# Optimization experiments

Hardware: AMD Instinct MI355X
Metric: run time of the kernel (lower is better)

The kernel has to match this reference:

```python
import jax, jax.numpy as jnp
import numpy as np

K = 5
BN_EPS = 1e-5


def _knn(xyz1, xyz2, embedding_lens):
    # squared pairwise distances [B, N, S]
    d2 = (jnp.sum(xyz1 ** 2, -1)[:, :, None]
          + jnp.sum(xyz2 ** 2, -1)[:, None, :]
          - 2.0 * jnp.einsum('bnc,bsc->bns', xyz1, xyz2))
    S = xyz2.shape[1]
    valid2 = jnp.arange(S)[None, :] < embedding_lens[:, None]  # [B, S]
    d2 = jnp.where(valid2[:, None, :], d2, jnp.float32(1e10))
    neg, idx = jax.lax.top_k(-d2, K)  # K smallest distances
    return -neg, idx  # squared dists [B,N,K], indices [B,N,K]


def _masked_bn(x, mask_f, gamma, beta):
    # x: [B, N, C]; mask_f: [B, N, 1] float; stats over valid positions only
    cnt = jnp.sum(mask_f)
    mean = jnp.sum(x * mask_f, axis=(0, 1)) / cnt
    var = jnp.sum(((x - mean) ** 2) * mask_f, axis=(0, 1)) / cnt
    return (x - mean) * jax.lax.rsqrt(var + BN_EPS) * gamma + beta


def setup_inputs() -> dict:
    key = jax.random.key(0)
    ks = jax.random.split(key, 8)
    B, N, S, D1, D2 = 16, 2048, 512, 384, 384
    xyz1 = jax.random.normal(ks[0], (B, N, 3), jnp.float32)
    xyz2 = jax.random.normal(ks[1], (B, S, 3), jnp.float32)
    points1 = jax.random.normal(ks[2], (B, N, D1), jnp.float32)
    points2 = jax.random.normal(ks[3], (B, S, D2), jnp.float32)
    point_lens = jax.random.randint(ks[4], (B,), N // 2, N + 1).astype(jnp.int32)
    embedding_lens = jax.random.randint(ks[5], (B,), S // 2, S + 1).astype(jnp.int32)
    point_mask = jnp.arange(N)[None, :] < point_lens[:, None]  # [B, N] bool
    Cin = D1 + D2
    W0 = jax.random.normal(ks[6], (768, Cin), jnp.float32) * (1.0 / np.sqrt(Cin))
    W1 = jax.random.normal(ks[7], (384, 768), jnp.float32) * (1.0 / np.sqrt(768))
    return dict(xyz1=xyz1, xyz2=xyz2, points1=points1, points2=points2,
                point_lens=point_lens, embedding_lens=embedding_lens,
                point_mask=point_mask,
                W0=W0, g0=jnp.ones((768,), jnp.float32), b0=jnp.zeros((768,), jnp.float32),
                W1=W1, g1=jnp.ones((384,), jnp.float32), b1=jnp.zeros((384,), jnp.float32))


def reference(xyz1, xyz2, points1, points2, point_lens, embedding_lens,
              point_mask, W0, g0, b0, W1, g1, b1):
    B, N, _ = xyz1.shape
    D2 = points2.shape[-1]
    dists, idx = _knn(xyz1[..., :3], xyz2, embedding_lens)
    eps = jnp.finfo(dists.dtype).eps
    dist_recip = 1.0 / (dists + eps)                    # [B, N, K]
    weight = dist_recip / jnp.sum(dist_recip, axis=2, keepdims=True)
    # masked gather: points2[b, idx[b,n,k], :] -> [B, N, K, D2]
    gathered = jnp.take_along_axis(points2, idx.reshape(B, N * K)[..., None],
                                   axis=1).reshape(B, N, K, D2)
    interp = jnp.sum(gathered * weight[..., None], axis=2)  # [B, N, D2]
    x = jnp.concatenate([points1, interp], axis=-1)          # [B, N, D1+D2]
    mask_f = point_mask.astype(x.dtype)[..., None]           # [B, N, 1]
    for W, g, b in ((W0, g0, b0), (W1, g1, b1)):
        x = jnp.einsum('bnc,dc->bnd', x, W)  # 1x1 conv, no bias
        x = jax.nn.relu(_masked_bn(x, mask_f, g, b))
    return x
```

## Files before the change

### kernel.cpp

```cpp
#include <hip/hip_runtime.h>
#include <cstdint>
#include <cstddef>

typedef unsigned short u16;
typedef __bf16 bf16x8 __attribute__((ext_vector_type(8)));
typedef float    f32x4 __attribute__((ext_vector_type(4)));
typedef unsigned int u32x4 __attribute__((ext_vector_type(4)));

constexpr int BB   = 16;
constexpr int NN   = 2048;
constexpr int SS   = 512;
constexpr int DD   = 384;
constexpr int CIN  = 768;
constexpr int HID  = 768;
constexpr int OUTC = 384;
constexpr int MROWS = BB * NN;
constexpr float KNN_EPS = 1.1920929e-07f;
constexpr float BN_EPS  = 1e-5f;

constexpr size_t OFF_W0B  = 0;
constexpr size_t OFF_W1B  = OFF_W0B  + (size_t)HID*CIN*2;
constexpr size_t OFF_IDX  = OFF_W1B  + (size_t)OUTC*HID*2;
constexpr size_t OFF_WGT  = OFF_IDX  + (size_t)MROWS*5*4;
constexpr size_t OFF_SUM1 = OFF_WGT  + (size_t)MROWS*5*4;
constexpr size_t OFF_SUM2 = OFF_SUM1 + (size_t)HID*2*4;
constexpr size_t OFF_COEF1= OFF_SUM2 + (size_t)OUTC*2*4;
constexpr size_t OFF_COEF2= OFF_COEF1+ (size_t)HID*2*4;
constexpr size_t OFF_XCAT = OFF_COEF2+ (size_t)OUTC*2*4;
constexpr size_t OFF_H1   = OFF_XCAT + (size_t)MROWS*CIN*2;

__device__ inline float bf2f(u16 u){ unsigned int i = ((unsigned int)u)<<16; float f; __builtin_memcpy(&f,&i,4); return f; }
__device__ inline u16 f2bf(float f){ unsigned int x; __builtin_memcpy(&x,&f,4);
  unsigned int r = (x + 0x7fffu + ((x>>16)&1u)) >> 16; return (u16)r; }

__device__ inline void async16(const void* g, void* l){
  __builtin_amdgcn_global_load_lds((const __attribute__((address_space(1))) void*)g,
                                   (__attribute__((address_space(3))) void*)l, 16, 0, 0);
}

__global__ void cvtw_kernel(const float* __restrict__ W0, const float* __restrict__ W1,
                            u16* __restrict__ W0b, u16* __restrict__ W1b){
  int t = blockIdx.x*256 + threadIdx.x;
  if (t < HID*CIN)  W0b[t] = f2bf(W0[t]);
  if (t < OUTC*HID) W1b[t] = f2bf(W1[t]);
}

__global__ __launch_bounds__(256) void knn_kernel(const float* __restrict__ xyz1,
                                                  const float* __restrict__ xyz2,
                                                  const int* __restrict__ elens,
                                                  int* __restrict__ idxO, float* __restrict__ wO){
  __shared__ f32x4 sp[SS];
  const int tid = threadIdx.x;
  const int wv = tid >> 6, lane = tid & 63;
  const int wg = blockIdx.x*4 + wv;
  const int b = wg >> 11;
  const int n = wg & (NN-1);
  for (int s = tid; s < SS; s += 256){
    float x = xyz2[((size_t)b*SS + s)*3 + 0];
    float y = xyz2[((size_t)b*SS + s)*3 + 1];
    float z = xyz2[((size_t)b*SS + s)*3 + 2];
    f32x4 v; v[0]=x; v[1]=y; v[2]=z; v[3]=x*x+y*y+z*z;
    sp[s]=v;
  }
  __syncthreads();
  const size_t qoff = ((size_t)b*NN + n)*3;
  const float qx = xyz1[qoff+0], qy = xyz1[qoff+1], qz = xyz1[qoff+2];
  const float qq = qx*qx + qy*qy + qz*qz;
  const int Sl = elens[b];

  float d0=1e30f,d1=1e30f,d2v=1e30f,d3=1e30f,d4=1e30f;
  int   i0=0,i1=0,i2=0,i3=0,i4=0;
  #pragma unroll
  for (int j=0;j<8;j++){
    const int s = lane + j*64;
    f32x4 v = sp[s];
    float d = (s < Sl) ? (qq + v[3] - 2.f*(qx*v[0] + qy*v[1] + qz*v[2])) : 1e30f;
    bool lt4=d<d4, lt3=d<d3, lt2=d<d2v, lt1=d<d1, lt0=d<d0;
    float nd4 = lt3 ? d3 : (lt4 ? d : d4); int ni4 = lt3 ? i3 : (lt4 ? s : i4);
    float nd3 = lt2 ? d2v: (lt3 ? d : d3); int ni3 = lt2 ? i2 : (lt3 ? s : i3);
    float nd2 = lt1 ? d1 : (lt2 ? d : d2v);int ni2 = lt1 ? i1 : (lt2 ? s : i2);
    float nd1 = lt0 ? d0 : (lt1 ? d : d1); int ni1 = lt0 ? i0 : (lt1 ? s : i1);
    float nd0 = lt0 ? d  : d0;             int ni0 = lt0 ? s  : i0;
    d4=nd4;i4=ni4; d3=nd3;i3=ni3; d2v=nd2;i2=ni2; d1=nd1;i1=ni1; d0=nd0;i0=ni0;
  }
  float outd[5]; int outi[5];
  #pragma unroll
  for (int r=0;r<5;r++){
    float bd = d0; int bs = i0;
    #pragma unroll
    for (int m=1;m<64;m<<=1){
      float od = __shfl_xor(bd, m, 64);
      int   os = __shfl_xor(bs, m, 64);
      if (od < bd || (od == bd && os < bs)){ bd = od; bs = os; }
    }
    outd[r]=bd; outi[r]=bs;
    if (d0 == bd && i0 == bs){ d0=d1;i0=i1; d1=d2v;i1=i2; d2v=d3;i2=i3; d3=d4;i3=i4; d4=1e30f;i4=0; }
  }
  if (lane == 0){
    float r0=1.f/(outd[0]+KNN_EPS), r1=1.f/(outd[1]+KNN_EPS), r2=1.f/(outd[2]+KNN_EPS),
          r3=1.f/(outd[3]+KNN_EPS), r4=1.f/(outd[4]+KNN_EPS);
    float inv = 1.f/(r0+r1+r2+r3+r4);
    size_t base = (size_t)wg*5;
    idxO[base+0]=outi[0]; idxO[base+1]=outi[1]; idxO[base+2]=outi[2]; idxO[base+3]=outi[3]; idxO[base+4]=outi[4];
    wO[base+0]=r0*inv; wO[base+1]=r1*inv; wO[base+2]=r2*inv; wO[base+3]=r3*inv; wO[base+4]=r4*inv;
  }
}

__global__ __launch_bounds__(384) void xcat_kernel(const float* __restrict__ p1,
                                                   const float* __restrict__ p2,
                                                   const int* __restrict__ idx,
                                                   const float* __restrict__ wgt,
                                                   u16* __restrict__ xcat){
  const int c = threadIdx.x;
  const int rowbase = blockIdx.x*8;
  for (int i=0;i<8;i++){
    const int row = rowbase + i;
    const int b = row >> 11;
    float v1 = p1[(size_t)row*DD + c];
    xcat[(size_t)row*CIN + c] = f2bf(v1);
    float acc = 0.f;
    size_t ib = (size_t)row*5;
    #pragma unroll
    for (int k=0;k<5;k++){
      int id = idx[ib+k]; float w = wgt[ib+k];
      acc += w * p2[((size_t)b*SS + id)*DD + c];
    }
    xcat[(size_t)row*CIN + DD + c] = f2bf(acc);
  }
}

template<bool OUT_BF16, int GX>
__global__ __launch_bounds__(256, 4) void gemm8p_kernel(const u16* __restrict__ A,
                                                        const u16* __restrict__ Bw,
                                                        void* __restrict__ Cout,
                                                        const int* __restrict__ plen,
                                                        float* __restrict__ sums){
  constexpr int K   = 768;
  constexpr int NC  = GX*128;
  constexpr int NT  = K/32;
  constexpr int NWG = GX*256;
  constexpr int CPX = NWG/8;
  __shared__ u16 Ash[2][128*32];
  __shared__ u16 Bsh[2][128*32];
  const int tid  = threadIdx.x;
  const int lane = tid & 63, wv = tid >> 6;
  const int wr = wv >> 1, wc = wv & 1;
  const int l15 = lane & 15, l16 = lane >> 4;
  const int swz = (l15 >> 1) & 3;

  const int logical = (blockIdx.x & 7)*CPX + (blockIdx.x >> 3);
  const int bn = logical % GX, bm = logical / GX;

  const int srow = tid >> 2;
  const int sk4  = (tid & 3) ^ ((tid >> 3) & 3);
  const u16* gA = A  + (size_t)(bm*128 + srow)*K + sk4*8;
  const u16* gB = Bw + (size_t)(bn*128 + srow)*K + sk4*8;
  const int dst0 = (wv*64)*16;
  const int dst1 = (256 + wv*64)*16;

  auto stageA = [&](int tt, int bi){
    async16(gA + tt*32,        (char*)&Ash[bi][0] + dst0);
    async16(gA + tt*32 + 64*K, (char*)&Ash[bi][0] + dst1);
  };
  auto stageB = [&](int tt, int bi){
    async16(gB + tt*32,        (char*)&Bsh[bi][0] + dst0);
    async16(gB + tt*32 + 64*K, (char*)&Bsh[bi][0] + dst1);
  };

  int aoff[4], boff[4];
  #pragma unroll
  for (int m=0;m<4;m++) aoff[m] = (wr*64 + m*16 + l15)*32 + ((l16 ^ swz) << 3);
  #pragma unroll
  for (int n=0;n<4;n++) boff[n] = (wc*64 + n*16 + l15)*32 + ((l16 ^ swz) << 3);

  f32x4 acc[4][4] = {};

  stageA(0,0); stageB(0,0); stageA(1,1); stageB(1,1);
  asm volatile("s_waitcnt vmcnt(4)" ::: "memory");
  __builtin_amdgcn_s_barrier();
  __builtin_amdgcn_sched_barrier(0);

  for (int t=0; t<NT; ++t){
    const int cur = t & 1;
    const int tt = (t+2 < NT) ? (t+2) : (NT-1);
    bf16x8 af0 = *reinterpret_cast<const bf16x8*>(&Ash[cur][aoff[0]]);
    bf16x8 af1 = *reinterpret_cast<const bf16x8*>(&Ash[cur][aoff[1]]);
    bf16x8 af2 = *reinterpret_cast<const bf16x8*>(&Ash[cur][aoff[2]]);
    bf16x8 af3 = *reinterpret_cast<const bf16x8*>(&Ash[cur][aoff[3]]);
    bf16x8 bv0 = *reinterpret_cast<const bf16x8*>(&Bsh[cur][boff[0]]);
    bf16x8 bv1 = *reinterpret_cast<const bf16x8*>(&Bsh[cur][boff[1]]);
    asm volatile("s_waitcnt lgkmcnt(0)" ::: "memory");
    __builtin_amdgcn_s_barrier();
    __builtin_amdgcn_sched_barrier(0);
    stageA(tt, cur);
    __builtin_amdgcn_s_setprio(1);
    acc[0][0] = __builtin_amdgcn_mfma_f32_16x16x32_bf16(af0, bv0, acc[0][0], 0,0,0);
    acc[1][0] = __builtin_amdgcn_mfma_f32_16x16x32_bf16(af1, bv0, acc[1][0], 0,0,0);
    acc[2][0] = __builtin_amdgcn_mfma_f32_16x16x32_bf16(af2, bv0, acc[2][0], 0,0,0);
    acc[3][0] = __builtin_amdgcn_mfma_f32_16x16x32_bf16(af3, bv0, acc[3][0], 0,0,0);
    acc[0][1] = __builtin_amdgcn_mfma_f32_16x16x32_bf16(af0, bv1, acc[0][1], 0,0,0);
    acc[1][1] = __builtin_amdgcn_mfma_f32_16x16x32_bf16(af1, bv1, acc[1][1], 0,0,0);
    acc[2][1] = __builtin_amdgcn_mfma_f32_16x16x32_bf16(af2, bv1, acc[2][1], 0,0,0);
    acc[3][1] = __builtin_amdgcn_mfma_f32_16x16x32_bf16(af3, bv1, acc[3][1], 0,0,0);
    __builtin_amdgcn_s_setprio(0);
    bf16x8 bv2 = *reinterpret_cast<const bf16x8*>(&Bsh[cur][boff[2]]);
    bf16x8 bv3 = *reinterpret_cast<const bf16x8*>(&Bsh[cur][boff[3]]);
    asm volatile("s_waitcnt lgkmcnt(0)" ::: "memory");
    __builtin_amdgcn_s_barrier();
    __builtin_amdgcn_sched_barrier(0);
    stageB(tt, cur);
    __builtin_amdgcn_s_setprio(1);
    acc[0][2] = __builtin_amdgcn_mfma_f32_16x16x32_bf16(af0, bv2, acc[0][2], 0,0,0);
    acc[1][2] = __builtin_amdgcn_mfma_f32_16x16x32_bf16(af1, bv2, acc[1][2], 0,0,0);
    acc[2][2] = __builtin_amdgcn_mfma_f32_16x16x32_bf16(af2, bv2, acc[2][2], 0,0,0);
    acc[3][2] = __builtin_amdgcn_mfma_f32_16x16x32_bf16(af3, bv2, acc[3][2], 0,0,0);
    acc[0][3] = __builtin_amdgcn_mfma_f32_16x16x32_bf16(af0, bv3, acc[0][3], 0,0,0);
    acc[1][3] = __builtin_amdgcn_mfma_f32_16x16x32_bf16(af1, bv3, acc[1][3], 0,0,0);
    acc[2][3] = __builtin_amdgcn_mfma_f32_16x16x32_bf16(af2, bv3, acc[2][3], 0,0,0);
    acc[3][3] = __builtin_amdgcn_mfma_f32_16x16x32_bf16(af3, bv3, acc[3][3], 0,0,0);
    __builtin_amdgcn_s_setprio(0);
    asm volatile("s_waitcnt vmcnt(4)" ::: "memory");
    __builtin_amdgcn_s_barrier();
    __builtin_amdgcn_sched_barrier(0);
  }
  asm volatile("s_waitcnt vmcnt(0)" ::: "memory");
  __syncthreads();

  #pragma unroll
  for (int m=0;m<4;m++){
    int r0 = bm*128 + wr*64 + m*16 + l16*4;
    #pragma unroll
    for (int n=0;n<4;n++){
      int c = bn*128 + wc*64 + n*16 + l15;
      #pragma unroll
      for (int r=0;r<4;r++){
        size_t off = (size_t)(r0+r)*NC + c;
        if (OUT_BF16) ((u16*)Cout)[off] = f2bf(acc[m][n][r]);
        else          ((float*)Cout)[off] = acc[m][n][r];
      }
    }
  }

  const int pl = plen[bm >> 4];
  const int rbase = (bm & 15)*128 + wr*64 + l16*4;
  float cs[4] = {0.f,0.f,0.f,0.f}, cs2[4] = {0.f,0.f,0.f,0.f};
  #pragma unroll
  for (int m=0;m<4;m++){
    #pragma unroll
    for (int r=0;r<4;r++){
      if (rbase + m*16 + r < pl){
        #pragma unroll
        for (int n=0;n<4;n++){
          float v = acc[m][n][r];
          cs[n] += v; cs2[n] += v*v;
        }
      }
    }
  }
  #pragma unroll
  for (int n=0;n<4;n++){
    cs[n]  += __shfl_xor(cs[n], 16, 64);  cs[n]  += __shfl_xor(cs[n], 32, 64);
    cs2[n] += __shfl_xor(cs2[n], 16, 64); cs2[n] += __shfl_xor(cs2[n], 32, 64);
  }
  float* lsum = (float*)&Ash[0][0];
  lsum[tid] = 0.f;
  __syncthreads();
  if (l16 == 0){
    #pragma unroll
    for (int n=0;n<4;n++){
      int col = wc*64 + n*16 + l15;
      atomicAdd(&lsum[col], cs[n]);
      atomicAdd(&lsum[128 + col], cs2[n]);
    }
  }
  __syncthreads();
  if (tid < 128)       atomicAdd(&sums[bn*128 + tid], lsum[tid]);
  else                 atomicAdd(&sums[NC + bn*128 + (tid-128)], lsum[tid]);
}

__global__ void coef_kernel(const float* __restrict__ sums, const int* __restrict__ plen,
                            const float* __restrict__ g, const float* __restrict__ bta,
                            float* __restrict__ coef, int C){
  int c = threadIdx.x;
  if (c >= C) return;
  float cnt = 0.f;
  for (int b=0;b<BB;b++) cnt += (float)plen[b];
  float mean = sums[c] / cnt;
  float var  = sums[C + c] / cnt - mean*mean;
  var = fmaxf(var, 0.f);
  float a = g[c] * rsqrtf(var + BN_EPS);
  coef[c] = a;
  coef[C + c] = bta[c] - mean*a;
}

__global__ __launch_bounds__(256) void bnrelu_kernel(const u16* __restrict__ H,
                                                     const float* __restrict__ coef,
                                                     u16* __restrict__ Z){
  size_t t = (size_t)blockIdx.x*256 + threadIdx.x;
  size_t f = t*8;
  int c = (int)(f % (size_t)HID);
  u32x4 v = *reinterpret_cast<const u32x4*>(H + f);
  u32x4 o;
  #pragma unroll
  for (int j=0;j<4;j++){
    float lo = bf2f((u16)(v[j] & 0xffffu));
    float hi = bf2f((u16)(v[j] >> 16));
    lo = fmaxf(lo*coef[c+2*j]   + coef[HID+c+2*j],   0.f);
    hi = fmaxf(hi*coef[c+2*j+1] + coef[HID+c+2*j+1], 0.f);
    o[j] = (unsigned int)f2bf(lo) | ((unsigned int)f2bf(hi) << 16);
  }
  *reinterpret_cast<u32x4*>(Z + f) = o;
}

__global__ __launch_bounds__(256) void final_kernel(float* __restrict__ Y,
                                                    const float* __restrict__ coef){
  size_t t = (size_t)blockIdx.x*256 + threadIdx.x;
  size_t f = t*4;
  int c = (int)(f % (size_t)OUTC);
  f32x4 v = *reinterpret_cast<const f32x4*>(Y + f);
  #pragma unroll
  for (int j=0;j<4;j++)
    v[j] = fmaxf(v[j]*coef[c+j] + coef[OUTC+c+j], 0.f);
  *reinterpret_cast<f32x4*>(Y + f) = v;
}

extern "C" void kernel_launch(void* const* d_in, const int* in_sizes, int n_in,
                              void* d_out, int out_size, void* d_ws, size_t ws_size,
                              hipStream_t stream){
  (void)in_sizes; (void)n_in; (void)out_size; (void)ws_size;
  const float* xyz1 = (const float*)d_in[0];
  const float* xyz2 = (const float*)d_in[1];
  const float* p1   = (const float*)d_in[2];
  const float* p2   = (const float*)d_in[3];
  const int*   plen = (const int*)d_in[4];
  const int*   elen = (const int*)d_in[5];
  const float* W0   = (const float*)d_in[7];
  const float* g0   = (const float*)d_in[8];
  const float* b0   = (const float*)d_in[9];
  const float* W1   = (const float*)d_in[10];
  const float* g1   = (const float*)d_in[11];
  const float* b1   = (const float*)d_in[12];
  float* out = (float*)d_out;
  char*  ws  = (char*)d_ws;

  u16*   W0b  = (u16*)  (ws + OFF_W0B);
  u16*   W1b  = (u16*)  (ws + OFF_W1B);
  int*   idxb = (int*)  (ws + OFF_IDX);
  float* wgtb = (float*)(ws + OFF_WGT);
  float* sum1 = (float*)(ws + OFF_SUM1);
  float* sum2 = (float*)(ws + OFF_SUM2);
  float* coef1= (float*)(ws + OFF_COEF1);
  float* coef2= (float*)(ws + OFF_COEF2);
  u16*   xcat = (u16*)  (ws + OFF_XCAT);
  u16*   h1   = (u16*)  (ws + OFF_H1);

  hipMemsetAsync(ws + OFF_SUM1, 0, (size_t)(HID*2 + OUTC*2)*4, stream);

  cvtw_kernel<<<(HID*CIN + 255)/256, 256, 0, stream>>>(W0, W1, W0b, W1b);
  knn_kernel<<<MROWS/4, 256, 0, stream>>>(xyz1, xyz2, elen, idxb, wgtb);
  xcat_kernel<<<MROWS/8, 384, 0, stream>>>(p1, p2, idxb, wgtb, xcat);

  gemm8p_kernel<true, 6><<<6*256, 256, 0, stream>>>(xcat, W0b, h1, plen, sum1);
  coef_kernel<<<1, HID, 0, stream>>>(sum1, plen, g0, b0, coef1, HID);

  bnrelu_kernel<<<(size_t)MROWS*HID/8/256, 256, 0, stream>>>(h1, coef1, xcat);

  gemm8p_kernel<false, 3><<<3*256, 256, 0, stream>>>(xcat, W1b, out, plen, sum2);
  coef_kernel<<<1, OUTC, 0, stream>>>(sum2, plen, g1, b1, coef2, OUTC);
  final_kernel<<<(size_t)MROWS*OUTC/4/256, 256, 0, stream>>>(out, coef2);
}
```

Before: 196.9 us.

## Fuse BN+ReLU of first layer into second GEMM's A-tile loading

Removes the standalone bnrelu pass over the 32768x768 hidden tensor. The second GEMM now loads A through registers, applies the per-channel scale/shift and ReLU, and writes the result to shared memory, while B is still staged asynchronously. This saves a full read and write of the bf16 hidden activations. In exchange the A path becomes a register round-trip with extra VALU work inside the pipelined loop. The first GEMM also gets its own specialization with launch bounds raised to 5 waves.

Result: slower. 231.2 us (+17.4%).

```diff
diff --git a/kernel.cpp b/kernel.cpp
--- a/kernel.cpp
+++ b/kernel.cpp
@@ -129,14 +129,14 @@
   }
 }
 
-template<bool OUT_BF16, int GX>
-__global__ __launch_bounds__(256, 4) void gemm8p_kernel(const u16* __restrict__ A,
-                                                        const u16* __restrict__ Bw,
-                                                        void* __restrict__ Cout,
-                                                        const int* __restrict__ plen,
-                                                        float* __restrict__ sums){
-  constexpr int K   = 768;
-  constexpr int NC  = GX*128;
+__global__ __launch_bounds__(256, 5) void gemm1_kernel(const u16* __restrict__ A,
+                                                       const u16* __restrict__ Bw,
+                                                       u16* __restrict__ Cout,
+                                                       const int* __restrict__ plen,
+                                                       float* __restrict__ sums){
+  constexpr int K   = CIN;
+  constexpr int NC  = HID;
+  constexpr int GX  = NC/128;
   constexpr int NT  = K/32;
   constexpr int NWG = GX*256;
   constexpr int CPX = NWG/8;
@@ -233,11 +233,8 @@
     for (int n=0;n<4;n++){
       int c = bn*128 + wc*64 + n*16 + l15;
       #pragma unroll
-      for (int r=0;r<4;r++){
-        size_t off = (size_t)(r0+r)*NC + c;
-        if (OUT_BF16) ((u16*)Cout)[off] = f2bf(acc[m][n][r]);
-        else          ((float*)Cout)[off] = acc[m][n][r];
-      }
+      for (int r=0;r<4;r++)
+        Cout[(size_t)(r0+r)*NC + c] = f2bf(acc[m][n][r]);
     }
   }
 
@@ -293,23 +290,189 @@
   coef[C + c] = bta[c] - mean*a;
 }
 
-__global__ __launch_bounds__(256) void bnrelu_kernel(const u16* __restrict__ H,
-                                                     const float* __restrict__ coef,
-                                                     u16* __restrict__ Z){
-  size_t t = (size_t)blockIdx.x*256 + threadIdx.x;
-  size_t f = t*8;
-  int c = (int)(f % (size_t)HID);
-  u32x4 v = *reinterpret_cast<const u32x4*>(H + f);
-  u32x4 o;
-  #pragma unroll
-  for (int j=0;j<4;j++){
-    float lo = bf2f((u16)(v[j] & 0xffffu));
-    float hi = bf2f((u16)(v[j] >> 16));
-    lo = fmaxf(lo*coef[c+2*j]   + coef[HID+c+2*j],   0.f);
-    hi = fmaxf(hi*coef[c+2*j+1] + coef[HID+c+2*j+1], 0.f);
-    o[j] = (unsigned int)f2bf(lo) | ((unsigned int)f2bf(hi) << 16);
-  }
-  *reinterpret_cast<u32x4*>(Z + f) = o;
+__global__ __launch_bounds__(256, 4) void gemm2f_kernel(const u16* __restrict__ A,
+                                                        const u16* __restrict__ Bw,
+                                                        float* __restrict__ Cout,
+                                                        const int* __restrict__ plen,
+                                                        float* __restrict__ sums,
+                                                        const float* __restrict__ cf){
+  constexpr int K   = HID;
+  constexpr int NC  = OUTC;
+  constexpr int GX  = NC/128;
+  constexpr int NT  = K/32;
+  constexpr int NWG = (MROWS/128)*GX;
+  constexpr int CPX = NWG/8;
+  __shared__ u16 Ash[2][4096];
+  __shared__ u16 Bsh[2][4096];
+  const int tid  = threadIdx.x;
+  const int lane = tid & 63, wv = tid >> 6;
+  const int wr = wv >> 1, wc = wv & 1;
+  const int l15 = lane & 15, l16 = lane >> 4;
+  const int swz = (l15 >> 1) & 3;
+
+  const int logical = (blockIdx.x & 7)*CPX + (blockIdx.x >> 3);
+  const int bn = logical % GX, bm = logical / GX;
+
+  const int srow = tid >> 2;
+  const int sk4  = (tid & 3) ^ ((tid >> 3) & 3);
+  const u16* gB  = Bw + (size_t)(bn*128 + srow)*K + sk4*8;
+  const u16* gA0 = A  + (size_t)(bm*128 + srow)*K + sk4*8;
+  const u16* gA1 = gA0 + (size_t)64*K;
+
+  const int dst0 = (wv*64)*16;
+  const int dst1 = (256 + wv*64)*16;
+  auto stageB = [&](int tt, int bi){
+    async16(gB + tt*32,        (char*)&Bsh[bi][0] + dst0);
+    async16(gB + tt*32 + 64*K, (char*)&Bsh[bi][0] + dst1);
+  };
+
+  u32x4 ha0, ha1, hb0, hb1;
+  auto loadA = [&](int tt, u32x4& r0, u32x4& r1){
+    r0 = *reinterpret_cast<const u32x4*>(gA0 + tt*32);
+    r1 = *reinterpret_cast<const u32x4*>(gA1 + tt*32);
+  };
+  auto bnw1 = [&](int nb, int tt, const u32x4& v, int uoff){
+    const int k0 = tt*32 + sk4*8;
+    float av[8], bv[8];
+    *reinterpret_cast<f32x4*>(av)   = *reinterpret_cast<const f32x4*>(cf + k0);
+    *reinterpret_cast<f32x4*>(av+4) = *reinterpret_cast<const f32x4*>(cf + k0 + 4);
+    *reinterpret_cast<f32x4*>(bv)   = *reinterpret_cast<const f32x4*>(cf + K + k0);
+    *reinterpret_cast<f32x4*>(bv+4) = *reinterpret_cast<const f32x4*>(cf + K + k0 + 4);
+    u32x4 o;
+    #pragma unroll
+    for (int q=0;q<4;q++){
+      float lo = bf2f((u16)(v[q] & 0xffffu));
+      float hi = bf2f((u16)(v[q] >> 16));
+      lo = fmaxf(lo*av[2*q]   + bv[2*q],   0.f);
+      hi = fmaxf(hi*av[2*q+1] + bv[2*q+1], 0.f);
+      o[q] = (unsigned int)f2bf(lo) | ((unsigned int)f2bf(hi) << 16);
+    }
+    *reinterpret_cast<u32x4*>(&Ash[nb][uoff]) = o;
+  };
+  auto bnwrite = [&](int nb, int tt, const u32x4& v0, const u32x4& v1){
+    bnw1(nb, tt, v0, tid*8);
+    bnw1(nb, tt, v1, 2048 + tid*8);
+  };
+
+  int aoff[4], boff[4];
+  #pragma unroll
+  for (int m=0;m<4;m++) aoff[m] = (wr*64 + m*16 + l15)*32 + ((l16 ^ swz) << 3);
+  #pragma unroll
+  for (int n=0;n<4;n++) boff[n] = (wc*64 + n*16 + l15)*32 + ((l16 ^ swz) << 3);
+
+  f32x4 acc[4][4] = {};
+
+  loadA(0, ha0, ha1);
+  stageB(0, 0);
+  __builtin_amdgcn_sched_barrier(0);
+  bnwrite(0, 0, ha0, ha1);
+  __builtin_amdgcn_sched_barrier(0);
+  loadA(1, hb0, hb1);
+  __builtin_amdgcn_sched_barrier(0);
+  asm volatile("s_waitcnt vmcnt(2)" ::: "memory");
+  asm volatile("s_waitcnt lgkmcnt(0)" ::: "memory");
+  __builtin_amdgcn_s_barrier();
+  __builtin_amdgcn_sched_barrier(0);
+
+  auto tile = [&](int t, int cur, const u32x4& c0v, const u32x4& c1v, u32x4& n0v, u32x4& n1v){
+    const int nxt = cur ^ 1;
+    const int t1 = (t+1 < NT) ? (t+1) : (NT-1);
+    const int t2 = (t+2 < NT) ? (t+2) : (NT-1);
+    const u16* Ac = &Ash[cur][0];
+    const u16* Bc = &Bsh[cur][0];
+    bf16x8 af0 = *reinterpret_cast<const bf16x8*>(Ac + aoff[0]);
+    bf16x8 af1 = *reinterpret_cast<const bf16x8*>(Ac + aoff[1]);
+    bf16x8 af2 = *reinterpret_cast<const bf16x8*>(Ac + aoff[2]);
+    bf16x8 af3 = *reinterpret_cast<const bf16x8*>(Ac + aoff[3]);
+    bf16x8 bv0 = *reinterpret_cast<const bf16x8*>(Bc + boff[0]);
+    bf16x8 bv1 = *reinterpret_cast<const bf16x8*>(Bc + boff[1]);
+    bf16x8 bv2 = *reinterpret_cast<const bf16x8*>(Bc + boff[2]);
+    bf16x8 bv3 = *reinterpret_cast<const bf16x8*>(Bc + boff[3]);
+    stageB(t1, nxt);
+    __builtin_amdgcn_sched_barrier(0);
+    loadA(t2, n0v, n1v);
+    __builtin_amdgcn_sched_barrier(0);
+    asm volatile("s_waitcnt lgkmcnt(0)" ::: "memory");
+    __builtin_amdgcn_sched_barrier(0);
+    __builtin_amdgcn_s_setprio(1);
+    acc[0][0] = __builtin_amdgcn_mfma_f32_16x16x32_bf16(af0, bv0, acc[0][0], 0,0,0);
+    acc[1][0] = __builtin_amdgcn_mfma_f32_16x16x32_bf16(af1, bv0, acc[1][0], 0,0,0);
+    acc[2][0] = __builtin_amdgcn_mfma_f32_16x16x32_bf16(af2, bv0, acc[2][0], 0,0,0);
+    acc[3][0] = __builtin_amdgcn_mfma_f32_16x16x32_bf16(af3, bv0, acc[3][0], 0,0,0);
+    acc[0][1] = __builtin_amdgcn_mfma_f32_16x16x32_bf16(af0, bv1, acc[0][1], 0,0,0);
+    acc[1][1] = __builtin_amdgcn_mfma_f32_16x16x32_bf16(af1, bv1, acc[1][1], 0,0,0);
+    acc[2][1] = __builtin_amdgcn_mfma_f32_16x16x32_bf16(af2, bv1, acc[2][1], 0,0,0);
+    acc[3][1] = __builtin_amdgcn_mfma_f32_16x16x32_bf16(af3, bv1, acc[3][1], 0,0,0);
+    acc[0][2] = __builtin_amdgcn_mfma_f32_16x16x32_bf16(af0, bv2, acc[0][2], 0,0,0);
+    acc[1][2] = __builtin_amdgcn_mfma_f32_16x16x32_bf16(af1, bv2, acc[1][2], 0,0,0);
+    acc[2][2] = __builtin_amdgcn_mfma_f32_16x16x32_bf16(af2, bv2, acc[2][2], 0,0,0);
+    acc[3][2] = __builtin_amdgcn_mfma_f32_16x16x32_bf16(af3, bv2, acc[3][2], 0,0,0);
+    acc[0][3] = __builtin_amdgcn_mfma_f32_16x16x32_bf16(af0, bv3, acc[0][3], 0,0,0);
+    acc[1][3] = __builtin_amdgcn_mfma_f32_16x16x32_bf16(af1, bv3, acc[1][3], 0,0,0);
+    acc[2][3] = __builtin_amdgcn_mfma_f32_16x16x32_bf16(af2, bv3, acc[2][3], 0,0,0);
+    acc[3][3] = __builtin_amdgcn_mfma_f32_16x16x32_bf16(af3, bv3, acc[3][3], 0,0,0);
+    __builtin_amdgcn_s_setprio(0);
+    bnwrite(nxt, t1, c0v, c1v);
+    asm volatile("s_waitcnt vmcnt(2)" ::: "memory");
+    asm volatile("s_waitcnt lgkmcnt(0)" ::: "memory");
+    __builtin_amdgcn_s_barrier();
+    __builtin_amdgcn_sched_barrier(0);
+  };
+
+  for (int t=0; t<NT; t+=2){
+    tile(t,   0, hb0, hb1, ha0, ha1);
+    tile(t+1, 1, ha0, ha1, hb0, hb1);
+  }
+  asm volatile("s_waitcnt vmcnt(0)" ::: "memory");
+  __syncthreads();
+
+  #pragma unroll
+  for (int m=0;m<4;m++){
+    int r0 = bm*128 + wr*64 + m*16 + l16*4;
+    #pragma unroll
+    for (int n=0;n<4;n++){
+      int c = bn*128 + wc*64 + n*16 + l15;
+      #pragma unroll
+      for (int r=0;r<4;r++)
+        Cout[(size_t)(r0+r)*NC + c] = acc[m][n][r];
+    }
+  }
+
+  const int pl = plen[bm >> 4];
+  const int rbase = (bm & 15)*128 + wr*64 + l16*4;
+  float cs[4] = {0.f,0.f,0.f,0.f}, cs2[4] = {0.f,0.f,0.f,0.f};
+  #pragma unroll
+  for (int m=0;m<4;m++){
+    #pragma unroll
+    for (int r=0;r<4;r++){
+      if (rbase + m*16 + r < pl){
+        #pragma unroll
+        for (int n=0;n<4;n++){
+          float v = acc[m][n][r];
+          cs[n] += v; cs2[n] += v*v;
+        }
+      }
+    }
+  }
+  #pragma unroll
+  for (int n=0;n<4;n++){
+    cs[n]  += __shfl_xor(cs[n], 16, 64);  cs[n]  += __shfl_xor(cs[n], 32, 64);
+    cs2[n] += __shfl_xor(cs2[n], 16, 64); cs2[n] += __shfl_xor(cs2[n], 32, 64);
+  }
+  float* lsum = (float*)&Ash[0][0];
+  lsum[tid] = 0.f;
+  __syncthreads();
+  if (l16 == 0){
+    #pragma unroll
+    for (int n=0;n<4;n++){
+      int col = wc*64 + n*16 + l15;
+      atomicAdd(&lsum[col], cs[n]);
+      atomicAdd(&lsum[128 + col], cs2[n]);
+    }
+  }
+  __syncthreads();
+  if (tid < 128)       atomicAdd(&sums[bn*128 + tid], lsum[tid]);
+  else                 atomicAdd(&sums[NC + bn*128 + (tid-128)], lsum[tid]);
 }
 
 __global__ __launch_bounds__(256) void final_kernel(float* __restrict__ Y,
@@ -360,12 +523,10 @@
   knn_kernel<<<MROWS/4, 256, 0, stream>>>(xyz1, xyz2, elen, idxb, wgtb);
   xcat_kernel<<<MROWS/8, 384, 0, stream>>>(p1, p2, idxb, wgtb, xcat);
 
-  gemm8p_kernel<true, 6><<<6*256, 256, 0, stream>>>(xcat, W0b, h1, plen, sum1);
+  gemm1_kernel<<<6*256, 256, 0, stream>>>(xcat, W0b, h1, plen, sum1);
   coef_kernel<<<1, HID, 0, stream>>>(sum1, plen, g0, b0, coef1, HID);
 
-  bnrelu_kernel<<<(size_t)MROWS*HID/8/256, 256, 0, stream>>>(h1, coef1, xcat);
-
-  gemm8p_kernel<false, 3><<<3*256, 256, 0, stream>>>(xcat, W1b, out, plen, sum2);
+  gemm2f_kernel<<<3*256, 256, 0, stream>>>(h1, W1b, out, plen, sum2, coef1);
   coef_kernel<<<1, OUTC, 0, stream>>>(sum2, plen, g1, b1, coef2, OUTC);
   final_kernel<<<(size_t)MROWS*OUTC/4/256, 256, 0, stream>>>(out, coef2);
 }
```
